# Optimization experiments

Measured on AMD Instinct MI355X. Metric: run time of the kernel, lower is better.

The kernel has to match this reference:

```python
import jax, jax.numpy as jnp
import numpy as np

UNITS = 64
T = 100


def setup_inputs() -> dict:
    key = jax.random.key(0)
    ks = jax.random.split(key, 9)
    B, F = 16384, 3
    x = jax.random.normal(ks[0], (B, T, F), dtype=jnp.float32)
    # give each sequence a random valid length; zero the tail so Masking(0.0) kicks in
    lengths = jax.random.randint(ks[8], (B,), 20, T + 1)
    valid = (jnp.arange(T)[None, :] < lengths[:, None])  # (B, T) bool
    x = x * valid[:, :, None].astype(jnp.float32)
    s = 1.0 / np.sqrt(UNITS)
    return {
        "x": x,
        "W": jax.random.normal(ks[1], (F, 4 * UNITS), dtype=jnp.float32) * s,
        "U": jax.random.normal(ks[2], (UNITS, 4 * UNITS), dtype=jnp.float32) * s,
        "b": jax.random.normal(ks[3], (4 * UNITS,), dtype=jnp.float32) * 0.1,
        "W1": jax.random.normal(ks[4], (UNITS, 64), dtype=jnp.float32) * s,
        "b1": jnp.zeros((64,), dtype=jnp.float32),
        "W2": jax.random.normal(ks[5], (64, 5), dtype=jnp.float32) * s,
        "b2": jnp.zeros((5,), dtype=jnp.float32),
    }


def _masked_lstm(x, W, U, b):
    # x: (B, T, F). Keras Masking(0.0): step masked iff all features == 0.
    B = x.shape[0]
    mask = jnp.any(x != 0.0, axis=-1)                 # (B, T)
    xT = jnp.swapaxes(x, 0, 1)                        # (T, B, F)
    mT = jnp.swapaxes(mask, 0, 1)                     # (T, B)
    # precompute input projection for all steps: (T, B, 4U)
    zx = jnp.einsum('tbf,fg->tbg', xT, W) + b
    h0 = jnp.zeros((B, UNITS), dtype=x.dtype)
    c0 = jnp.zeros((B, UNITS), dtype=x.dtype)

    def step(carry, inp):
        h, c = carry
        zxt, mt = inp
        z = zxt + h @ U                               # (B, 4U)
        i, f, g, o = jnp.split(z, 4, axis=-1)         # Keras gate order i,f,c,o
        i = jax.nn.sigmoid(i)
        f = jax.nn.sigmoid(f)
        o = jax.nn.sigmoid(o)
        c_new = f * c + i * jnp.tanh(g)
        h_new = o * jnp.tanh(c_new)
        m = mt[:, None]
        h = jnp.where(m, h_new, h)                    # masked steps: carry state
        c = jnp.where(m, c_new, c)
        return (h, c), None

    (h, _), _ = jax.lax.scan(step, (h0, c0), (zx, mT))
    return h                                          # (B, UNITS) last carried output


def reference(x, W, U, b, W1, b1, W2, b2):
    h = _masked_lstm(x, W, U, b)
    h1 = jax.nn.relu(h @ W1 + b1)
    return jax.nn.softmax(h1 @ W2 + b2, axis=-1)      # (B, 5)
```

## Files before the change

### kernel.cpp

```cpp
#include <hip/hip_runtime.h>
#include <math.h>

#define UNITS 64
#define TT 100
#define NB 16
#define NTH 256
#define HSTR 72
#define XSTR 32

typedef _Float16 half8 __attribute__((ext_vector_type(8)));
typedef _Float16 half4 __attribute__((ext_vector_type(4)));
typedef float floatx4 __attribute__((ext_vector_type(4)));

#define LOG2E 1.44269504088896f

__device__ __forceinline__ float rcp_fast(float x) { return __builtin_amdgcn_rcpf(x); }
__device__ __forceinline__ float exp2_fast(float x) { return __builtin_amdgcn_exp2f(x); }

__device__ __forceinline__ float fast_sigmoid(float x) {
    return rcp_fast(1.0f + exp2_fast(-LOG2E * x));
}

__device__ __forceinline__ float fast_tanh(float x) {
    return __builtin_fmaf(2.0f, rcp_fast(1.0f + exp2_fast(-2.0f * LOG2E * x)), -1.0f);
}

__global__ __launch_bounds__(256) void len_kernel(
    const float* __restrict__ x, int* __restrict__ len, int B)
{
    const int row = blockIdx.x * 4 + (threadIdx.x >> 6);
    const int l = threadIdx.x & 63;
    if (row >= B) return;
    const float* xp = x + (size_t)row * (TT * 3);
    int m = 0;
    #pragma unroll
    for (int t = l; t < TT; t += 64) {
        const float a = xp[3 * t], b = xp[3 * t + 1], c = xp[3 * t + 2];
        if (a != 0.0f || b != 0.0f || c != 0.0f) m = t + 1;
    }
    #pragma unroll
    for (int off = 32; off; off >>= 1)
        m = max(m, __shfl_down(m, off, 64));
    if (l == 0) len[row] = m;
}

__global__ __launch_bounds__(256) void sort_kernel(
    const int* __restrict__ len, int* __restrict__ perm, int* __restrict__ rlen, int B)
{
    __shared__ int sh_hist[TT + 1];
    __shared__ int sh_base[TT + 1];
    const int tid = threadIdx.x;

    for (int i = tid; i <= TT; i += 256) sh_hist[i] = 0;
    __syncthreads();
    for (int b = tid; b < B; b += 256) atomicAdd(&sh_hist[len[b]], 1);
    __syncthreads();
    if (tid <= TT) {
        int s = 0;
        for (int k = tid + 1; k <= TT; ++k) s += sh_hist[k];
        sh_base[tid] = s;
    }
    __syncthreads();
    for (int b = tid; b < B; b += 256) {
        const int l = len[b];
        const int r = sh_base[l] + atomicAdd(&sh_hist[l], -1) - 1;
        if (r >= 0 && r < B) { perm[r] = b; rlen[r] = l; }
    }
}

__global__ __launch_bounds__(NTH, 4) void lstm_mfma_kernel(
    const float* __restrict__ x,
    const float* __restrict__ W,
    const float* __restrict__ U,
    const float* __restrict__ bias,
    const float* __restrict__ W1,
    const float* __restrict__ b1,
    const float* __restrict__ W2,
    const float* __restrict__ b2,
    const int*   __restrict__ perm,
    const int*   __restrict__ rlen,
    float* __restrict__ out,
    int B)
{
    __shared__ __align__(16) _Float16 hbuf[NB * HSTR];
    __shared__ __align__(16) _Float16 xh[NB * XSTR];
    __shared__ float maskbuf[NB];
    __shared__ float h1buf[NB * 64];
    __shared__ float logitbuf[NB * 5];

    const int tid = threadIdx.x;
    const int w   = tid >> 6;
    const int l   = tid & 63;
    const int q   = l >> 4;
    const int cnl = l & 15;
    const int b0  = blockIdx.x * NB;

    int maxlen = rlen ? rlen[b0] : TT;
    maxlen = (maxlen < 0) ? 0 : ((maxlen > TT) ? TT : maxlen);

    int gb = b0 + tid;
    if (perm && tid < NB) gb = perm[b0 + tid];
    gb = (gb < 0) ? 0 : ((gb >= B) ? (B - 1) : gb);
    const float* xrow = x + (size_t)gb * (TT * 3);

    half8 Bf[4][3];
    #pragma unroll
    for (int g = 0; g < 4; ++g) {
        const int zc = 64 * g + 16 * w + cnl;
        #pragma unroll
        for (int kb = 0; kb < 3; ++kb)
            #pragma unroll
            for (int j = 0; j < 8; ++j) {
                const int k = 32 * kb + 8 * q + j;
                float v = 0.0f;
                if (k < 64)       v = U[k * 256 + zc];
                else if (k < 67)  v = W[(k - 64) * 256 + zc];
                else if (k == 67) v = bias[zc];
                Bf[g][kb][j] = (_Float16)v;
            }
    }

    for (int i = tid; i < NB * HSTR; i += NTH) hbuf[i] = (_Float16)0.0f;
    for (int i = tid; i < NB * XSTR; i += NTH) xh[i] = (_Float16)0.0f;
    float c4[4] = {0.0f, 0.0f, 0.0f, 0.0f};
    const floatx4 zero4 = {0.0f, 0.0f, 0.0f, 0.0f};

    float px0 = 0.0f, px1 = 0.0f, px2 = 0.0f;
    if (tid < NB) { px0 = xrow[0]; px1 = xrow[1]; px2 = xrow[2]; }
    __syncthreads();

    #pragma unroll 1
    for (int t = 0; t < maxlen; ++t) {
        if (tid < NB) {
            half4 xv4 = { (_Float16)px0, (_Float16)px1, (_Float16)px2, (_Float16)1.0f };
            *(half4*)&xh[tid * XSTR] = xv4;
            maskbuf[tid] = (px0 != 0.0f || px1 != 0.0f || px2 != 0.0f) ? 1.0f : 0.0f;
        }
        __syncthreads();

        const half8 A0 = *(const half8*)&hbuf[cnl * HSTR + 8 * q];
        const half8 A1 = *(const half8*)&hbuf[cnl * HSTR + 32 + 8 * q];
        const half8 AX = *(const half8*)&xh[cnl * XSTR + 8 * q];

        float msk[4];
        #pragma unroll
        for (int r = 0; r < 4; ++r) msk[r] = maskbuf[4 * q + r];

        if (tid < NB) {
            const int tp = (t + 1 < TT) ? (t + 1) : (TT - 1);
            const float* xp = xrow + 3 * tp;
            px0 = xp[0]; px1 = xp[1]; px2 = xp[2];
        }

        floatx4 acc[4];
        #pragma unroll
        for (int g = 0; g < 4; ++g) {
            acc[g] = __builtin_amdgcn_mfma_f32_16x16x32_f16(AX, Bf[g][2], zero4, 0, 0, 0);
            acc[g] = __builtin_amdgcn_mfma_f32_16x16x32_f16(A0, Bf[g][0], acc[g], 0, 0, 0);
            acc[g] = __builtin_amdgcn_mfma_f32_16x16x32_f16(A1, Bf[g][1], acc[g], 0, 0, 0);
        }

        _Float16 hnew[4];
        #pragma unroll
        for (int r = 0; r < 4; ++r) {
            const float iv = fast_sigmoid(acc[0][r]);
            const float fv = fast_sigmoid(acc[1][r]);
            const float gv = fast_tanh  (acc[2][r]);
            const float ov = fast_sigmoid(acc[3][r]);
            const float cn = fv * c4[r] + iv * gv;
            c4[r] = (msk[r] != 0.0f) ? cn : c4[r];
            hnew[r] = (_Float16)(ov * fast_tanh(cn));
        }

        __syncthreads();
        #pragma unroll
        for (int r = 0; r < 4; ++r)
            if (msk[r] != 0.0f)
                hbuf[(4 * q + r) * HSTR + 16 * w + cnl] = hnew[r];
    }
    __syncthreads();

    {
        const int j  = tid & 63;
        const int bb = tid >> 6;
        const float bj = b1[j];
        #pragma unroll
        for (int p = 0; p < NB / 4; ++p) {
            const int b = p * 4 + bb;
            float acc = bj;
            #pragma unroll 8
            for (int k = 0; k < UNITS; ++k)
                acc += (float)hbuf[b * HSTR + k] * W1[k * 64 + j];
            h1buf[b * 64 + j] = fmaxf(acc, 0.0f);
        }
    }
    __syncthreads();

    if (tid < NB * 5) {
        const int b = tid / 5, s = tid % 5;
        float acc = b2[s];
        for (int j = 0; j < 64; ++j)
            acc += h1buf[b * 64 + j] * W2[j * 5 + s];
        logitbuf[b * 5 + s] = acc;
    }
    __syncthreads();

    if (tid < NB) {
        const float l0 = logitbuf[tid * 5 + 0];
        const float l1 = logitbuf[tid * 5 + 1];
        const float l2 = logitbuf[tid * 5 + 2];
        const float l3 = logitbuf[tid * 5 + 3];
        const float l4 = logitbuf[tid * 5 + 4];
        const float m  = fmaxf(fmaxf(fmaxf(l0, l1), fmaxf(l2, l3)), l4);
        const float e0 = __expf(l0 - m), e1 = __expf(l1 - m), e2 = __expf(l2 - m);
        const float e3 = __expf(l3 - m), e4 = __expf(l4 - m);
        const float rs = 1.0f / (e0 + e1 + e2 + e3 + e4);
        out[(size_t)gb * 5 + 0] = e0 * rs;
        out[(size_t)gb * 5 + 1] = e1 * rs;
        out[(size_t)gb * 5 + 2] = e2 * rs;
        out[(size_t)gb * 5 + 3] = e3 * rs;
        out[(size_t)gb * 5 + 4] = e4 * rs;
    }
}

extern "C" void kernel_launch(void* const* d_in, const int* in_sizes, int n_in,
                              void* d_out, int out_size, void* d_ws, size_t ws_size,
                              hipStream_t stream) {
    const float* x  = (const float*)d_in[0];
    const float* W  = (const float*)d_in[1];
    const float* U  = (const float*)d_in[2];
    const float* b  = (const float*)d_in[3];
    const float* W1 = (const float*)d_in[4];
    const float* b1 = (const float*)d_in[5];
    const float* W2 = (const float*)d_in[6];
    const float* b2 = (const float*)d_in[7];
    float* out = (float*)d_out;

    const int B = in_sizes[0] / (TT * 3);

    const size_t need = (size_t)3 * B * sizeof(int);
    int* perm = nullptr; int* rlen = nullptr;

    if (ws_size >= need) {
        int* len = (int*)d_ws;
        perm     = len + B;
        rlen     = perm + B;
        len_kernel<<<dim3((B + 3) / 4), dim3(256), 0, stream>>>(x, len, B);
        sort_kernel<<<dim3(1), dim3(256), 0, stream>>>(len, perm, rlen, B);
    }

    lstm_mfma_kernel<<<dim3(B / NB), dim3(NTH), 0, stream>>>(
        x, W, U, b, W1, b1, W2, b2, perm, rlen, out, B);
}
```

Before: 223.7 us.

## Fuse length sort into cooperative LSTM kernel and double-buffer hidden state

Folds the length-scan and counting-sort kernels into the LSTM kernel, launched cooperatively with grid-wide syncs, falling back to the old multi-kernel path if the launch fails. Each block now stages its whole input sequence into LDS as fp16 before the recurrence. It also ping-pongs the hidden-state buffer, which removes one block barrier per timestep. The per-step mask becomes a comparison against the precomputed per-row length instead of a per-step zero check. The aim is to cut launch overhead, per-step global loads and barriers, at the cost of grid syncs and reliance on all blocks being co-resident.

```diff
diff --git a/kernel.cpp b/kernel.cpp
--- a/kernel.cpp
+++ b/kernel.cpp
@@ -1,12 +1,15 @@
 #include <hip/hip_runtime.h>
+#include <hip/hip_cooperative_groups.h>
 #include <math.h>
+
+namespace cg = cooperative_groups;
 
 #define UNITS 64
 #define TT 100
 #define NB 16
 #define NTH 256
 #define HSTR 72
-#define XSTR 32
+#define XQSTR 18
 
 typedef _Float16 half8 __attribute__((ext_vector_type(8)));
 typedef _Float16 half4 __attribute__((ext_vector_type(4)));
@@ -20,7 +23,6 @@
 __device__ __forceinline__ float fast_sigmoid(float x) {
     return rcp_fast(1.0f + exp2_fast(-LOG2E * x));
 }
-
 __device__ __forceinline__ float fast_tanh(float x) {
     return __builtin_fmaf(2.0f, rcp_fast(1.0f + exp2_fast(-2.0f * LOG2E * x)), -1.0f);
 }
@@ -33,14 +35,12 @@
     if (row >= B) return;
     const float* xp = x + (size_t)row * (TT * 3);
     int m = 0;
+    for (int t = l; t < TT; t += 64) {
+        const float a = xp[3*t], b = xp[3*t+1], c = xp[3*t+2];
+        if (a != 0.0f || b != 0.0f || c != 0.0f) m = t + 1;
+    }
     #pragma unroll
-    for (int t = l; t < TT; t += 64) {
-        const float a = xp[3 * t], b = xp[3 * t + 1], c = xp[3 * t + 2];
-        if (a != 0.0f || b != 0.0f || c != 0.0f) m = t + 1;
-    }
-    #pragma unroll
-    for (int off = 32; off; off >>= 1)
-        m = max(m, __shfl_down(m, off, 64));
+    for (int off = 32; off; off >>= 1) m = max(m, __shfl_down(m, off, 64));
     if (l == 0) len[row] = m;
 }
 
@@ -50,7 +50,6 @@
     __shared__ int sh_hist[TT + 1];
     __shared__ int sh_base[TT + 1];
     const int tid = threadIdx.x;
-
     for (int i = tid; i <= TT; i += 256) sh_hist[i] = 0;
     __syncthreads();
     for (int b = tid; b < B; b += 256) atomicAdd(&sh_hist[len[b]], 1);
@@ -68,7 +67,7 @@
     }
 }
 
-__global__ __launch_bounds__(NTH, 4) void lstm_mfma_kernel(
+__global__ __launch_bounds__(NTH, 4) void lstm_coop_kernel(
     const float* __restrict__ x,
     const float* __restrict__ W,
     const float* __restrict__ U,
@@ -77,31 +76,90 @@
     const float* __restrict__ b1,
     const float* __restrict__ W2,
     const float* __restrict__ b2,
-    const int*   __restrict__ perm,
-    const int*   __restrict__ rlen,
-    float* __restrict__ out,
-    int B)
+    int* __restrict__ len, int* __restrict__ perm, int* __restrict__ rlen,
+    int* __restrict__ hist, int* __restrict__ cursor, int* __restrict__ offs,
+    float* __restrict__ out, int B, int do_sort)
 {
-    __shared__ __align__(16) _Float16 hbuf[NB * HSTR];
-    __shared__ __align__(16) _Float16 xh[NB * XSTR];
-    __shared__ float maskbuf[NB];
+    __shared__ __align__(16) _Float16 hb[2][NB * HSTR];
+    __shared__ __align__(16) _Float16 xt[TT * XQSTR * 4];
+    __shared__ __align__(16) _Float16 zq[8];
+    __shared__ int shInt[128];
     __shared__ float h1buf[NB * 64];
     __shared__ float logitbuf[NB * 5];
+
+    cg::grid_group grid = cg::this_grid();
 
     const int tid = threadIdx.x;
     const int w   = tid >> 6;
     const int l   = tid & 63;
     const int q   = l >> 4;
     const int cnl = l & 15;
-    const int b0  = blockIdx.x * NB;
-
-    int maxlen = rlen ? rlen[b0] : TT;
+    const int bi  = blockIdx.x;
+    const int b0  = bi * NB;
+    const int grp = tid >> 4;
+    const int sub = tid & 15;
+
+    if (do_sort) {
+        {
+            const float* xp = x + (size_t)(b0 + grp) * (TT * 3);
+            int m = 0;
+            for (int t = sub; t < TT; t += 16) {
+                const float a = xp[3*t], b = xp[3*t+1], c = xp[3*t+2];
+                if (a != 0.0f || b != 0.0f || c != 0.0f) m = t + 1;
+            }
+            #pragma unroll
+            for (int off = 8; off; off >>= 1) m = max(m, __shfl_down(m, off, 16));
+            if (sub == 0) len[b0 + grp] = m;
+        }
+        if (bi == 0 && tid < 101) { hist[tid] = 0; cursor[tid] = 0; }
+        grid.sync();
+        if (tid < NB) atomicAdd(&hist[len[b0 + tid]], 1);
+        grid.sync();
+        if (bi == 0) {
+            if (tid < 101) shInt[tid] = hist[tid];
+            __syncthreads();
+            if (tid < 101) {
+                int s = 0;
+                for (int k = tid + 1; k <= TT; ++k) s += shInt[k];
+                offs[tid] = s;
+            }
+        }
+        grid.sync();
+        if (tid < NB) {
+            const int b = b0 + tid;
+            const int ll = len[b];
+            const int r = offs[ll] + atomicAdd(&cursor[ll], 1);
+            if (r >= 0 && r < B) { perm[r] = b; rlen[r] = ll; }
+        }
+        grid.sync();
+    }
+
+    __syncthreads();
+    if (tid < NB) {
+        int g = perm ? perm[b0 + tid] : (b0 + tid);
+        g = (g < 0) ? 0 : ((g >= B) ? (B - 1) : g);
+        shInt[tid] = g;
+        int ll = rlen ? rlen[b0 + tid] : TT;
+        shInt[NB + tid] = (ll < 0) ? 0 : ((ll > TT) ? TT : ll);
+    }
+    if (tid < 8) zq[tid] = (_Float16)0.0f;
+    for (int i = tid; i < NB * HSTR; i += NTH) hb[0][i] = (_Float16)0.0f;
+    __syncthreads();
+
+    int maxlen = shInt[NB];
     maxlen = (maxlen < 0) ? 0 : ((maxlen > TT) ? TT : maxlen);
-
-    int gb = b0 + tid;
-    if (perm && tid < NB) gb = perm[b0 + tid];
-    gb = (gb < 0) ? 0 : ((gb >= B) ? (B - 1) : gb);
-    const float* xrow = x + (size_t)gb * (TT * 3);
+    int rl[4];
+    #pragma unroll
+    for (int r = 0; r < 4; ++r) rl[r] = shInt[NB + 4*q + r];
+
+    {
+        const float* xp = x + (size_t)shInt[grp] * (TT * 3);
+        for (int t = sub; t < maxlen; t += 16) {
+            const float a = xp[3*t], b = xp[3*t+1], c = xp[3*t+2];
+            half4 v = { (_Float16)a, (_Float16)b, (_Float16)c, (_Float16)1.0f };
+            *(half4*)&xt[(t * XQSTR + grp) * 4] = v;
+        }
+    }
 
     half8 Bf[4][3];
     #pragma unroll
@@ -120,37 +178,23 @@
             }
     }
 
-    for (int i = tid; i < NB * HSTR; i += NTH) hbuf[i] = (_Float16)0.0f;
-    for (int i = tid; i < NB * XSTR; i += NTH) xh[i] = (_Float16)0.0f;
     float c4[4] = {0.0f, 0.0f, 0.0f, 0.0f};
+    _Float16 hcur[4] = {(_Float16)0.0f, (_Float16)0.0f, (_Float16)0.0f, (_Float16)0.0f};
     const floatx4 zero4 = {0.0f, 0.0f, 0.0f, 0.0f};
 
-    float px0 = 0.0f, px1 = 0.0f, px2 = 0.0f;
-    if (tid < NB) { px0 = xrow[0]; px1 = xrow[1]; px2 = xrow[2]; }
     __syncthreads();
 
     #pragma unroll 1
     for (int t = 0; t < maxlen; ++t) {
-        if (tid < NB) {
-            half4 xv4 = { (_Float16)px0, (_Float16)px1, (_Float16)px2, (_Float16)1.0f };
-            *(half4*)&xh[tid * XSTR] = xv4;
-            maskbuf[tid] = (px0 != 0.0f || px1 != 0.0f || px2 != 0.0f) ? 1.0f : 0.0f;
-        }
-        __syncthreads();
-
-        const half8 A0 = *(const half8*)&hbuf[cnl * HSTR + 8 * q];
-        const half8 A1 = *(const half8*)&hbuf[cnl * HSTR + 32 + 8 * q];
-        const half8 AX = *(const half8*)&xh[cnl * XSTR + 8 * q];
-
-        float msk[4];
-        #pragma unroll
-        for (int r = 0; r < 4; ++r) msk[r] = maskbuf[4 * q + r];
-
-        if (tid < NB) {
-            const int tp = (t + 1 < TT) ? (t + 1) : (TT - 1);
-            const float* xp = xrow + 3 * tp;
-            px0 = xp[0]; px1 = xp[1]; px2 = xp[2];
-        }
+        const _Float16* hbc = hb[t & 1];
+        _Float16*       hbn = hb[(t + 1) & 1];
+
+        const half8 A0 = *(const half8*)&hbc[cnl * HSTR + 8 * q];
+        const half8 A1 = *(const half8*)&hbc[cnl * HSTR + 32 + 8 * q];
+        const _Float16* xaddr = (q == 0) ? &xt[(t * XQSTR + cnl) * 4] : zq;
+        const half4 x4 = *(const half4*)xaddr;
+        const half8 AX = { x4[0], x4[1], x4[2], x4[3],
+                           (_Float16)0.0f, (_Float16)0.0f, (_Float16)0.0f, (_Float16)0.0f };
 
         floatx4 acc[4];
         #pragma unroll
@@ -160,25 +204,23 @@
             acc[g] = __builtin_amdgcn_mfma_f32_16x16x32_f16(A1, Bf[g][1], acc[g], 0, 0, 0);
         }
 
-        _Float16 hnew[4];
         #pragma unroll
         for (int r = 0; r < 4; ++r) {
+            const bool live = (t < rl[r]);
             const float iv = fast_sigmoid(acc[0][r]);
             const float fv = fast_sigmoid(acc[1][r]);
             const float gv = fast_tanh  (acc[2][r]);
             const float ov = fast_sigmoid(acc[3][r]);
             const float cn = fv * c4[r] + iv * gv;
-            c4[r] = (msk[r] != 0.0f) ? cn : c4[r];
-            hnew[r] = (_Float16)(ov * fast_tanh(cn));
-        }
-
+            c4[r] = live ? cn : c4[r];
+            const _Float16 hn = (_Float16)(ov * fast_tanh(cn));
+            hcur[r] = live ? hn : hcur[r];
+            hbn[(4 * q + r) * HSTR + 16 * w + cnl] = hcur[r];
+        }
         __syncthreads();
-        #pragma unroll
-        for (int r = 0; r < 4; ++r)
-            if (msk[r] != 0.0f)
-                hbuf[(4 * q + r) * HSTR + 16 * w + cnl] = hnew[r];
-    }
-    __syncthreads();
+    }
+
+    const _Float16* hbL = hb[maxlen & 1];
 
     {
         const int j  = tid & 63;
@@ -190,7 +232,7 @@
             float acc = bj;
             #pragma unroll 8
             for (int k = 0; k < UNITS; ++k)
-                acc += (float)hbuf[b * HSTR + k] * W1[k * 64 + j];
+                acc += (float)hbL[b * HSTR + k] * W1[k * 64 + j];
             h1buf[b * 64 + j] = fmaxf(acc, 0.0f);
         }
     }
@@ -206,6 +248,7 @@
     __syncthreads();
 
     if (tid < NB) {
+        const int gb = shInt[tid];
         const float l0 = logitbuf[tid * 5 + 0];
         const float l1 = logitbuf[tid * 5 + 1];
         const float l2 = logitbuf[tid * 5 + 2];
@@ -236,19 +279,42 @@
     const float* b2 = (const float*)d_in[7];
     float* out = (float*)d_out;
 
-    const int B = in_sizes[0] / (TT * 3);
-
-    const size_t need = (size_t)3 * B * sizeof(int);
-    int* perm = nullptr; int* rlen = nullptr;
-
-    if (ws_size >= need) {
-        int* len = (int*)d_ws;
-        perm     = len + B;
-        rlen     = perm + B;
-        len_kernel<<<dim3((B + 3) / 4), dim3(256), 0, stream>>>(x, len, B);
-        sort_kernel<<<dim3(1), dim3(256), 0, stream>>>(len, perm, rlen, B);
-    }
-
-    lstm_mfma_kernel<<<dim3(B / NB), dim3(NTH), 0, stream>>>(
-        x, W, U, b, W1, b1, W2, b2, perm, rlen, out, B);
-}
+    int B = in_sizes[0] / (TT * 3);
+
+    int* len = nullptr; int* perm = nullptr; int* rlen = nullptr;
+    int* hist = nullptr; int* cursor = nullptr; int* offs = nullptr;
+    const bool have_ws = ws_size >= ((size_t)3 * B + 384) * sizeof(int);
+    if (have_ws) {
+        len    = (int*)d_ws;
+        perm   = len + B;
+        rlen   = perm + B;
+        hist   = rlen + B;
+        cursor = hist + 128;
+        offs   = cursor + 128;
+    }
+
+    int do_sort = have_ws ? 1 : 0;
+    void* args[] = {
+        (void*)&x, (void*)&W, (void*)&U, (void*)&b,
+        (void*)&W1, (void*)&b1, (void*)&W2, (void*)&b2,
+        (void*)&len, (void*)&perm, (void*)&rlen,
+        (void*)&hist, (void*)&cursor, (void*)&offs,
+        (void*)&out, (void*)&B, (void*)&do_sort
+    };
+    hipError_t err = hipSuccess;
+    if (have_ws) {
+        err = hipLaunchCooperativeKernel((const void*)lstm_coop_kernel,
+                                         dim3(B / NB), dim3(NTH), args, 0, stream);
+    }
+    if (!have_ws || err != hipSuccess) {
+        int* fperm = nullptr; int* frlen = nullptr;
+        if (have_ws) {
+            len_kernel<<<dim3((B + 3) / 4), dim3(256), 0, stream>>>(x, len, B);
+            sort_kernel<<<dim3(1), dim3(256), 0, stream>>>(len, perm, rlen, B);
+            fperm = perm; frlen = rlen;
+        }
+        lstm_coop_kernel<<<dim3(B / NB), dim3(NTH), 0, stream>>>(
+            x, W, U, b, W1, b1, W2, b2,
+            nullptr, fperm, frlen, nullptr, nullptr, nullptr, out, B, 0);
+    }
+}
```

After: 596.0 us. 2.66x slower.
